# Optimization experiments

Measured on AMD Instinct MI355X. Metric: run time of the kernel, lower is better.

## Reference

```python
import jax, jax.numpy as jnp
import numpy as np

H = 1024      # hidden_size
L = 4         # num_layers
DI = 2 * H    # d_inner (expand=2)
N = 16        # d_state
K = 4         # d_conv
BATCH = 2
S = 1024
EPS = 1e-5


def _layernorm(x, g, b):
    mu = jnp.mean(x, axis=-1, keepdims=True)
    xc = x - mu
    var = jnp.mean(xc * xc, axis=-1, keepdims=True)
    return xc * jax.lax.rsqrt(var + EPS) * g + b


def _causal_dwconv(x, w, b):
    # x: [B,S,DI], w: [DI,K], b: [DI]. Torch Conv1d(pad=K-1, groups=DI) truncated to S == causal left-pad conv.
    xp = jnp.pad(x, ((0, 0), (K - 1, 0), (0, 0)))
    s = x.shape[1]
    y = sum(xp[:, k:k + s, :] * w[:, k] for k in range(K))
    return y + b


def _forward(hidden_states, in_norm_g, in_norm_b, ln_g, ln_b, in_proj_w,
             conv_w, conv_b, x_proj_w, dt_proj_w, dt_proj_b, D,
             mamba_ln_g, mamba_ln_b, out_proj_w, op1_w, op1_b, op2_w, op2_b):
    dtype = hidden_states.dtype
    A = -jnp.arange(1, N + 1, dtype=dtype)  # [N]; == -exp(log(arange)), identical across d_inner rows
    x = _layernorm(hidden_states, in_norm_g, in_norm_b)
    for l in range(L):
        res_x = x
        xn = _layernorm(x, ln_g[l], ln_b[l])
        xr = jnp.einsum('bsh,ph->bsp', xn, in_proj_w[l])           # [B,S,2*DI]
        x_inner, res = jnp.split(xr, 2, axis=-1)
        x_inner = jax.nn.silu(x_inner)
        for c in range(2):
            x_inner = jax.nn.silu(_causal_dwconv(x_inner, conv_w[l, c], conv_b[l, c]))
        proj = jnp.einsum('bsd,pd->bsp', x_inner, x_proj_w[l])     # [B,S,1+2N]
        dt_raw, Bm, Cm = proj[..., :1], proj[..., 1:1 + N], proj[..., 1 + N:]
        dt = jax.nn.softplus(dt_raw * dt_proj_w[l][:, 0] + dt_proj_b[l])  # [B,S,DI]

        def step(h, inp_t):
            dt_t, x_t, B_t, C_t = inp_t                      # [B,DI],[B,DI],[B,N],[B,N]
            h = h + dt_t[..., None] * (h * A + x_t[..., None] * B_t[:, None, :])
            y = jnp.einsum('bdn,bn->bd', h, C_t)
            return h, y

        h0 = jnp.zeros((x.shape[0], DI, N), dtype=dtype)
        xs = (dt.transpose(1, 0, 2), x_inner.transpose(1, 0, 2),
              Bm.transpose(1, 0, 2), Cm.transpose(1, 0, 2))
        _, ys = jax.lax.scan(step, h0, xs)                   # ys: [S,B,DI]
        y = ys.transpose(1, 0, 2)
        y = y + x_inner * D[l]
        y = _layernorm(y, mamba_ln_g[l], mamba_ln_b[l])
        y = y * jax.nn.sigmoid(res)
        x = res_x + jnp.einsum('bsd,hd->bsh', y, out_proj_w[l])
    out = jax.nn.gelu(x @ op1_w.T + op1_b, approximate=False) @ op2_w.T + op2_b
    return out + hidden_states


def setup_inputs() -> dict:
    key = jax.random.key(0)
    ks = jax.random.split(key, 10)
    rn = lambda k, shape, s: jax.random.normal(k, shape, dtype=jnp.float32) * s
    return {
        'hidden_states': rn(ks[0], (BATCH, S, H), 1.0),
        'in_norm_g': jnp.ones((H,), jnp.float32),
        'in_norm_b': jnp.zeros((H,), jnp.float32),
        'ln_g': jnp.ones((L, H), jnp.float32),
        'ln_b': jnp.zeros((L, H), jnp.float32),
        'in_proj_w': rn(ks[1], (L, 2 * DI, H), 0.02),
        'conv_w': rn(ks[2], (L, 2, DI, K), 0.2),
        'conv_b': jnp.zeros((L, 2, DI), jnp.float32),
        'x_proj_w': rn(ks[3], (L, 1 + 2 * N, DI), 0.02),
        'dt_proj_w': rn(ks[4], (L, DI, 1), 0.01),
        'dt_proj_b': jnp.full((L, DI), -4.0, jnp.float32),  # keeps dt small -> stable scan
        'D': jnp.ones((L, DI), jnp.float32),
        'mamba_ln_g': jnp.ones((L, DI), jnp.float32),
        'mamba_ln_b': jnp.zeros((L, DI), jnp.float32),
        'out_proj_w': rn(ks[5], (L, H, DI), 0.02),
        'op1_w': rn(ks[6], (H, H), 0.02),
        'op1_b': jnp.zeros((H,), jnp.float32),
        'op2_w': rn(ks[7], (H, H), 0.02),
        'op2_b': jnp.zeros((H,), jnp.float32),
    }


def reference(hidden_states, in_norm_g, in_norm_b, ln_g, ln_b, in_proj_w,
              conv_w, conv_b, x_proj_w, dt_proj_w, dt_proj_b, D,
              mamba_ln_g, mamba_ln_b, out_proj_w, op1_w, op1_b, op2_w, op2_b):
    return _forward(hidden_states, in_norm_g, in_norm_b, ln_g, ln_b, in_proj_w,
                    conv_w, conv_b, x_proj_w, dt_proj_w, dt_proj_b, D,
                    mamba_ln_g, mamba_ln_b, out_proj_w, op1_w, op1_b, op2_w, op2_b)
```

## Files before the change

### kernel.cpp

```cpp
#include <hip/hip_runtime.h>
#include <hip/hip_bf16.h>
#include <math.h>

constexpr int HDIM = 1024;
constexpr int LNUM = 4;
constexpr int DINNER = 2048;
constexpr int KCONV = 4;
constexpr int NB = 2;
constexpr int SLEN = 1024;
constexpr int TOK = NB * SLEN;
constexpr float LNEPS = 1e-5f;

constexpr int NCHUNK = 32;
constexpr int CLEN = SLEN / NCHUNK;
constexpr int PROW = 36;
constexpr int XPN = 48;
constexpr int XSPLIT = 8;
constexpr int CCH = 32;

typedef __attribute__((ext_vector_type(8))) short short8;
typedef __attribute__((ext_vector_type(4))) float f32x4;

__device__ __forceinline__ __hip_bfloat16 f2bf(float x) { return __float2bfloat16(x); }
__device__ __forceinline__ unsigned short f2bfu(float x) {
    __hip_bfloat16 h = __float2bfloat16(x);
    return *(unsigned short*)&h;
}
__device__ __forceinline__ float sigmoidf_(float x) { return 1.f / (1.f + __expf(-x)); }
__device__ __forceinline__ float siluf_(float x) { return x / (1.f + __expf(-x)); }
__device__ __forceinline__ float softplusf_(float x) { return (x > 20.f) ? x : log1pf(__expf(x)); }

__device__ __forceinline__ void cp16(const void* g, void* l) {
    __builtin_amdgcn_global_load_lds(
        (const __attribute__((address_space(1))) unsigned int*)g,
        (__attribute__((address_space(3))) unsigned int*)l, 16, 0, 0);
}

__global__ __launch_bounds__(256) void cvt_k(const float* __restrict__ in,
                                             __hip_bfloat16* __restrict__ out, int n4)
{
    const int i = blockIdx.x * 256 + threadIdx.x;
    if (i >= n4) return;
    float4 v = ((const float4*)in)[i];
    ushort4 o;
    o.x = f2bfu(v.x); o.y = f2bfu(v.y); o.z = f2bfu(v.z); o.w = f2bfu(v.w);
    ((ushort4*)out)[i] = o;
}

__global__ __launch_bounds__(256) void cvtwx_k(const float* __restrict__ in,
                                               __hip_bfloat16* __restrict__ out)
{
    const int i = blockIdx.x * 256 + threadIdx.x;
    if (i >= LNUM * XPN * DINNER / 4) return;
    const int e = i * 4;
    const int l = e / (XPN * DINNER);
    const int rem = e - l * XPN * DINNER;
    const int r = rem >> 11;
    const int col = rem & (DINNER - 1);
    ushort4 o;
    if (r < 33) {
        float4 v = *(const float4*)&in[(((size_t)l * 33 + r) << 11) + col];
        o.x = f2bfu(v.x); o.y = f2bfu(v.y); o.z = f2bfu(v.z); o.w = f2bfu(v.w);
    } else {
        o.x = o.y = o.z = o.w = 0;
    }
    ((ushort4*)out)[i] = o;
}

template<int MODE, int D>
__global__ __launch_bounds__(256) void ln_k(
    const float* __restrict__ in, const float* __restrict__ g, const float* __restrict__ b,
    float* __restrict__ outF, __hip_bfloat16* __restrict__ outB,
    const float* __restrict__ gate, int gstride)
{
    constexpr int EPT = D / 1024;
    const int t = blockIdx.x, tid = threadIdx.x;
    float4 v[EPT];
    float s1 = 0.f, s2 = 0.f;
#pragma unroll
    for (int i = 0; i < EPT; ++i) {
        const int idx = (tid + i * 256) * 4;
        float4 val = *(const float4*)&in[(size_t)t * D + idx];
        v[i] = val;
        s1 += val.x + val.y + val.z + val.w;
        s2 += val.x * val.x + val.y * val.y + val.z * val.z + val.w * val.w;
    }
#pragma unroll
    for (int off = 32; off; off >>= 1) { s1 += __shfl_down(s1, off); s2 += __shfl_down(s2, off); }
    __shared__ float rs[4], rq[4];
    const int w = tid >> 6, lane = tid & 63;
    if (lane == 0) { rs[w] = s1; rq[w] = s2; }
    __syncthreads();
    const float mu = (rs[0] + rs[1] + rs[2] + rs[3]) * (1.f / D);
    const float ms = (rq[0] + rq[1] + rq[2] + rq[3]) * (1.f / D);
    const float var = ms - mu * mu;
    const float rstd = rsqrtf((var > 0.f ? var : 0.f) + LNEPS);
#pragma unroll
    for (int i = 0; i < EPT; ++i) {
        const int idx = (tid + i * 256) * 4;
        const float4 gg = *(const float4*)&g[idx];
        const float4 bb = *(const float4*)&b[idx];
        float4 o;
        o.x = (v[i].x - mu) * rstd * gg.x + bb.x;
        o.y = (v[i].y - mu) * rstd * gg.y + bb.y;
        o.z = (v[i].z - mu) * rstd * gg.z + bb.z;
        o.w = (v[i].w - mu) * rstd * gg.w + bb.w;
        if (MODE == 2) {
            const float4 gt = *(const float4*)&gate[(size_t)t * gstride + idx];
            o.x *= sigmoidf_(gt.x); o.y *= sigmoidf_(gt.y);
            o.z *= sigmoidf_(gt.z); o.w *= sigmoidf_(gt.w);
        }
        if (MODE == 0) {
            ((float4*)outF)[((size_t)t * D + idx) >> 2] = o;
        } else {
            ushort4 u;
            u.x = f2bfu(o.x); u.y = f2bfu(o.y); u.z = f2bfu(o.z); u.w = f2bfu(o.w);
            ((ushort4*)outB)[((size_t)t * D + idx) >> 2] = u;
        }
    }
}

template<int EPI>
__global__ __launch_bounds__(256) void gemm_bt(
    const unsigned short* __restrict__ A, const unsigned short* __restrict__ B,
    int M, int N, int Kd,
    float* __restrict__ Cf, __hip_bfloat16* __restrict__ Cb,
    const float* __restrict__ bias, const float* __restrict__ res,
    float* __restrict__ Of)
{
    __shared__ __align__(16) unsigned short As[2][128 * 32];
    __shared__ __align__(16) unsigned short Bs[2][128 * 32];
    const int tid = threadIdx.x;
    const int m0 = blockIdx.x * 128, n0 = blockIdx.y * 128;
    const int klen = Kd / (int)gridDim.z;
    const int kstart = (int)blockIdx.z * klen;
    const int nK = klen >> 5;
    const int wave = tid >> 6, lane = tid & 63;
    const int wm = (wave & 1) * 64, wn = (wave >> 1) * 64;
    const int quad = lane >> 4, l16 = lane & 15;
    f32x4 acc[4][4];
#pragma unroll
    for (int i = 0; i < 4; ++i)
#pragma unroll
        for (int j = 0; j < 4; ++j) acc[i][j] = (f32x4){0.f, 0.f, 0.f, 0.f};

    const int r1 = tid >> 2, kc1 = (tid & 3) * 8;
    const int r2 = r1 + 64;

    {
        const int k0 = kstart;
        cp16(&A[(size_t)(m0 + r1) * Kd + k0 + kc1], &As[0][tid * 8]);
        cp16(&A[(size_t)(m0 + r2) * Kd + k0 + kc1], &As[0][(tid + 256) * 8]);
        cp16(&B[(size_t)(n0 + r1) * Kd + k0 + kc1], &Bs[0][tid * 8]);
        cp16(&B[(size_t)(n0 + r2) * Kd + k0 + kc1], &Bs[0][(tid + 256) * 8]);
    }
    for (int kk = 0; kk < nK; ++kk) {
        __syncthreads();
        if (kk + 1 < nK) {
            const int k0 = kstart + ((kk + 1) << 5);
            const int nb = (kk + 1) & 1;
            cp16(&A[(size_t)(m0 + r1) * Kd + k0 + kc1], &As[nb][tid * 8]);
            cp16(&A[(size_t)(m0 + r2) * Kd + k0 + kc1], &As[nb][(tid + 256) * 8]);
            cp16(&B[(size_t)(n0 + r1) * Kd + k0 + kc1], &Bs[nb][tid * 8]);
            cp16(&B[(size_t)(n0 + r2) * Kd + k0 + kc1], &Bs[nb][(tid + 256) * 8]);
        }
        const int cb = kk & 1;
        short8 af[4], bfm[4];
#pragma unroll
        for (int i = 0; i < 4; ++i) af[i]  = *(const short8*)&As[cb][(wm + i * 16 + l16) * 32 + quad * 8];
#pragma unroll
        for (int j = 0; j < 4; ++j) bfm[j] = *(const short8*)&Bs[cb][(wn + j * 16 + l16) * 32 + quad * 8];
#pragma unroll
        for (int i = 0; i < 4; ++i)
#pragma unroll
            for (int j = 0; j < 4; ++j)
                acc[i][j] = __builtin_amdgcn_mfma_f32_16x16x32_bf16(af[i], bfm[j], acc[i][j], 0, 0, 0);
    }

    const size_t zoff = (EPI == 1) ? (size_t)blockIdx.z * M * N : 0;
#pragma unroll
    for (int i = 0; i < 4; ++i)
#pragma unroll
        for (int j = 0; j < 4; ++j)
#pragma unroll
            for (int r = 0; r < 4; ++r) {
                const int row = m0 + wm + i * 16 + quad * 4 + r;
                const int col = n0 + wn + j * 16 + l16;
                const size_t off = (size_t)row * N + col;
                float vv = acc[i][j][r];
                if (EPI == 0) {
                    Cf[off] = vv;
                } else if (EPI == 1) {
                    Cf[zoff + off] = vv;
                } else if (EPI == 2) {
                    float z = vv + bias[col];
                    Cb[off] = f2bf(0.5f * z * (1.f + erff(z * 0.70710678118f)));
                } else {
                    Of[off] = vv + bias[col] + res[off];
                }
            }
}

__global__ __launch_bounds__(256) void xcomb_k(const float* __restrict__ part,
                                               float* __restrict__ x, int n4)
{
    const int i = blockIdx.x * 256 + threadIdx.x;
    if (i >= n4) return;
    float4 a = ((const float4*)part)[i];
    float4 b = ((const float4*)part)[i + n4];
    float4 v = ((const float4*)x)[i];
    v.x += a.x + b.x; v.y += a.y + b.y; v.z += a.z + b.z; v.w += a.w + b.w;
    ((float4*)x)[i] = v;
}

__global__ __launch_bounds__(256) void pcomb_k(const float* __restrict__ ppart,
                                               float* __restrict__ proj)
{
    const int idx = blockIdx.x * 256 + threadIdx.x;
    if (idx >= TOK * 33) return;
    const int t = idx / 33, p2 = idx - t * 33;
    float s = 0.f;
#pragma unroll
    for (int k = 0; k < XSPLIT; ++k)
        s += ppart[(size_t)k * TOK * XPN + (size_t)t * XPN + p2];
    proj[idx] = s;
}

__global__ __launch_bounds__(256) void conv2_fused(
    const float* __restrict__ xin, int in_stride,
    const float* __restrict__ cw, const float* __restrict__ cb, int layer,
    float* __restrict__ out, __hip_bfloat16* __restrict__ outb)
{
    const int d = blockIdx.x * 256 + threadIdx.x;
    const int s0 = blockIdx.y * CCH;
    const int b = blockIdx.z;
    float w1k[4], w2k[4];
#pragma unroll
    for (int k = 0; k < 4; ++k) {
        w1k[k] = cw[(((size_t)layer * 2 + 0) * DINNER + d) * KCONV + k];
        w2k[k] = cw[(((size_t)layer * 2 + 1) * DINNER + d) * KCONV + k];
    }
    const float b1 = cb[((size_t)layer * 2 + 0) * DINNER + d];
    const float b2 = cb[((size_t)layer * 2 + 1) * DINNER + d];
    const float* base = xin + (size_t)b * SLEN * in_stride + d;

    float xv[CCH + 6];
#pragma unroll
    for (int i = 0; i < CCH + 6; ++i) {
        const int s = s0 - 6 + i;
        const int sc = (s < 0) ? 0 : s;
        xv[i] = base[(size_t)sc * in_stride];
    }
#pragma unroll
    for (int i = 0; i < CCH + 6; ++i) {
        const int s = s0 - 6 + i;
        xv[i] = (s >= 0) ? siluf_(xv[i]) : 0.f;
    }
    float c1[CCH + 3];
#pragma unroll
    for (int i = 0; i < CCH + 3; ++i) {
        const int s = s0 - 3 + i;
        float t = fmaf(w1k[0], xv[i], fmaf(w1k[1], xv[i + 1],
                  fmaf(w1k[2], xv[i + 2], fmaf(w1k[3], xv[i + 3], b1))));
        c1[i] = (s >= 0) ? siluf_(t) : 0.f;
    }
    const size_t obase = (size_t)b * SLEN * DINNER + d;
#pragma unroll
    for (int j = 0; j < CCH; ++j) {
        float t2 = fmaf(w2k[0], c1[j], fmaf(w2k[1], c1[j + 1],
                   fmaf(w2k[2], c1[j + 2], fmaf(w2k[3], c1[j + 3], b2))));
        const float v = siluf_(t2);
        out[obase + (size_t)(s0 + j) * DINNER] = v;
        outb[obase + (size_t)(s0 + j) * DINNER] = f2bf(v);
    }
}

__global__ __launch_bounds__(256) void xproj_mfma(
    const unsigned short* __restrict__ A, const unsigned short* __restrict__ B,
    float* __restrict__ ppart)
{
    __shared__ __align__(16) unsigned short As[2][128 * 32];
    __shared__ __align__(16) unsigned short Bs[2][XPN * 32];
    const int tid = threadIdx.x;
    const int m0 = blockIdx.x * 128;
    const int k0base = blockIdx.y * (DINNER / XSPLIT);
    constexpr int nK = (DINNER / XSPLIT) >> 5;
    const int wave = tid >> 6, lane = tid & 63;
    const int wm = wave * 32;
    const int quad = lane >> 4, l16 = lane & 15;
    f32x4 acc[2][3];
#pragma unroll
    for (int i = 0; i < 2; ++i)
#pragma unroll
        for (int j = 0; j < 3; ++j) acc[i][j] = (f32x4){0.f, 0.f, 0.f, 0.f};

    const int r1 = tid >> 2, kc1 = (tid & 3) * 8;
    {
        const int k0 = k0base;
        cp16(&A[(size_t)(m0 + r1) * DINNER + k0 + kc1], &As[0][tid * 8]);
        cp16(&A[(size_t)(m0 + r1 + 64) * DINNER + k0 + kc1], &As[0][(tid + 256) * 8]);
        if (tid < XPN * 4)
            cp16(&B[(size_t)r1 * DINNER + k0 + kc1], &Bs[0][tid * 8]);
    }
    for (int kk = 0; kk < nK; ++kk) {
        __syncthreads();
        if (kk + 1 < nK) {
            const int k0 = k0base + ((kk + 1) << 5);
            const int nb = (kk + 1) & 1;
            cp16(&A[(size_t)(m0 + r1) * DINNER + k0 + kc1], &As[nb][tid * 8]);
            cp16(&A[(size_t)(m0 + r1 + 64) * DINNER + k0 + kc1], &As[nb][(tid + 256) * 8]);
            if (tid < XPN * 4)
                cp16(&B[(size_t)r1 * DINNER + k0 + kc1], &Bs[nb][tid * 8]);
        }
        const int cb = kk & 1;
        short8 af[2], bfm[3];
#pragma unroll
        for (int i = 0; i < 2; ++i) af[i]  = *(const short8*)&As[cb][(wm + i * 16 + l16) * 32 + quad * 8];
#pragma unroll
        for (int j = 0; j < 3; ++j) bfm[j] = *(const short8*)&Bs[cb][(j * 16 + l16) * 32 + quad * 8];
#pragma unroll
        for (int i = 0; i < 2; ++i)
#pragma unroll
            for (int j = 0; j < 3; ++j)
                acc[i][j] = __builtin_amdgcn_mfma_f32_16x16x32_bf16(af[i], bfm[j], acc[i][j], 0, 0, 0);
    }
    float* pp = ppart + (size_t)blockIdx.y * TOK * XPN;
#pragma unroll
    for (int i = 0; i < 2; ++i)
#pragma unroll
        for (int j = 0; j < 3; ++j) {
            const int col = j * 16 + l16;
#pragma unroll
            for (int r = 0; r < 4; ++r) {
                const int row = m0 + wm + i * 16 + quad * 4 + r;
                pp[(size_t)row * XPN + col] = acc[i][j][r];
            }
        }
}

__device__ __forceinline__ void load_proj_chunk(float* sp, const float* __restrict__ proj,
                                                int b, int c, int tid)
{
    const float* psrc = proj + ((size_t)b * SLEN + (size_t)c * CLEN) * 33;
    for (int i = tid; i < CLEN * 33; i += 256) {
        int s = i / 33, p = i - s * 33;
        sp[s * PROW + (p == 0 ? 32 : p - 1)] = psrc[i];
    }
}

__global__ __launch_bounds__(256) void scan_partA(
    const float* __restrict__ proj, const float* __restrict__ xin,
    const float* __restrict__ dtw, const float* __restrict__ dtb, int layer,
    float* __restrict__ hloc, float* __restrict__ cumA_g)
{
    __shared__ __align__(16) float sp[CLEN * PROW];
    const int tid = threadIdx.x;
    const int d = blockIdx.x * 256 + tid;
    const int c = blockIdx.y, b = blockIdx.z;
    load_proj_chunk(sp, proj, b, c, tid);
    const float w_ = dtw[(size_t)layer * DINNER + d];
    const float bb = dtb[(size_t)layer * DINNER + d];
    __syncthreads();
    float h[16], ca[16];
#pragma unroll
    for (int n = 0; n < 16; ++n) { h[n] = 0.f; ca[n] = 1.f; }
    const float* xrow = xin + ((size_t)b * SLEN + (size_t)c * CLEN) * DINNER + d;
    float xt_next = xrow[0];
    for (int s = 0; s < CLEN; ++s) {
        const float xt = xt_next;
        if (s + 1 < CLEN) xt_next = xrow[(size_t)(s + 1) * DINNER];
        const float* row = &sp[s * PROW];
        const float dt = softplusf_(fmaf(row[32], w_, bb));
        const float u = dt * xt;
#pragma unroll
        for (int n = 0; n < 16; ++n) {
            const float a = fmaf(dt, -(float)(n + 1), 1.f);
            h[n] = fmaf(h[n], a, u * row[n]);
            ca[n] *= a;
        }
    }
    const size_t base = (((size_t)b * NCHUNK + c) * 16) * DINNER + d;
#pragma unroll
    for (int n = 0; n < 16; ++n) {
        hloc[base + (size_t)n * DINNER] = h[n];
        cumA_g[base + (size_t)n * DINNER] = ca[n];
    }
}

__global__ __launch_bounds__(256) void scan_combine(
    const float* __restrict__ hloc, const float* __restrict__ cumA_g,
    float* __restrict__ hin)
{
    const int idx = blockIdx.x * 256 + threadIdx.x;
    const int d = idx & (DINNER - 1);
    const int n = (idx >> 11) & 15;
    const int b = idx >> 15;
    float h = 0.f;
    for (int c = 0; c < NCHUNK; ++c) {
        const size_t off = (((size_t)b * NCHUNK + c) * 16 + n) * DINNER + d;
        hin[off] = h;
        h = fmaf(cumA_g[off], h, hloc[off]);
    }
}

__global__ __launch_bounds__(256) void scan_partC(
    const float* __restrict__ proj, const float* __restrict__ xin,
    const float* __restrict__ dtw, const float* __restrict__ dtb,
    const float* __restrict__ Dp, int layer,
    const float* __restrict__ hin, float* __restrict__ y)
{
    __shared__ __align__(16) float sp[CLEN * PROW];
    const int tid = threadIdx.x;
    const int d = blockIdx.x * 256 + tid;
    const int c = blockIdx.y, b = blockIdx.z;
    load_proj_chunk(sp, proj, b, c, tid);
    const float w_ = dtw[(size_t)layer * DINNER + d];
    const float bb = dtb[(size_t)layer * DINNER + d];
    const float Dd = Dp[(size_t)layer * DINNER + d];
    __syncthreads();
    float h[16];
    const size_t base = (((size_t)b * NCHUNK + c) * 16) * DINNER + d;
#pragma unroll
    for (int n = 0; n < 16; ++n) h[n] = hin[base + (size_t)n * DINNER];
    const float* xrow = xin + ((size_t)b * SLEN + (size_t)c * CLEN) * DINNER + d;
    float* yrow = y + ((size_t)b * SLEN + (size_t)c * CLEN) * DINNER + d;
    float xt_next = xrow[0];
    for (int s = 0; s < CLEN; ++s) {
        const float xt = xt_next;
        if (s + 1 < CLEN) xt_next = xrow[(size_t)(s + 1) * DINNER];
        const float* row = &sp[s * PROW];
        const float dt = softplusf_(fmaf(row[32], w_, bb));
        const float u = dt * xt;
        float yp = 0.f;
#pragma unroll
        for (int n = 0; n < 16; ++n) {
            const float a = fmaf(dt, -(float)(n + 1), 1.f);
            h[n] = fmaf(h[n], a, u * row[n]);
            yp = fmaf(h[n], row[16 + n], yp);
        }
        yrow[(size_t)s * DINNER] = yp + xt * Dd;
    }
}

__global__ __launch_bounds__(256) void cast_f2b(const float* __restrict__ in,
                                                __hip_bfloat16* __restrict__ out, int n4)
{
    int i = blockIdx.x * 256 + threadIdx.x;
    if (i >= n4) return;
    float4 v = ((const float4*)in)[i];
    ushort4 u;
    u.x = f2bfu(v.x); u.y = f2bfu(v.y); u.z = f2bfu(v.z); u.w = f2bfu(v.w);
    ((ushort4*)out)[i] = u;
}

extern "C" void kernel_launch(void* const* d_in, const int* in_sizes, int n_in,
                              void* d_out, int out_size, void* d_ws, size_t ws_size,
                              hipStream_t stream)
{
    (void)in_sizes; (void)n_in; (void)out_size;
    const float* hs   = (const float*)d_in[0];
    const float* ing  = (const float*)d_in[1];
    const float* inb  = (const float*)d_in[2];
    const float* lng  = (const float*)d_in[3];
    const float* lnb  = (const float*)d_in[4];
    const float* ipw  = (const float*)d_in[5];
    const float* cw   = (const float*)d_in[6];
    const float* cbp  = (const float*)d_in[7];
    const float* xpw  = (const float*)d_in[8];
    const float* dtw  = (const float*)d_in[9];
    const float* dtb  = (const float*)d_in[10];
    const float* Dp   = (const float*)d_in[11];
    const float* mlg  = (const float*)d_in[12];
    const float* mlb  = (const float*)d_in[13];
    const float* opw  = (const float*)d_in[14];
    const float* w1f  = (const float*)d_in[15];
    const float* b1f  = (const float*)d_in[16];
    const float* w2f  = (const float*)d_in[17];
    const float* b2f  = (const float*)d_in[18];

    char* p = (char*)d_ws;
    float* x   = (float*)p; p += (size_t)TOK * HDIM * 4;
    float* xr  = (float*)p; p += (size_t)TOK * 2 * DINNER * 4;
    float* c2  = (float*)p; p += (size_t)TOK * DINNER * 4;
    float* yb  = (float*)p; p += (size_t)TOK * DINNER * 4;
    float* proj= (float*)p; p += ((size_t)TOK * 33 * 4 + 255) & ~(size_t)255;
    float* hin = (float*)p; p += (size_t)NB * NCHUNK * 16 * DINNER * 4;
    float* ppart=(float*)p; p += (size_t)XSPLIT * TOK * XPN * 4;
    __hip_bfloat16* xn  = (__hip_bfloat16*)p; p += (size_t)TOK * HDIM * 2;
    __hip_bfloat16* y2  = (__hip_bfloat16*)p; p += (size_t)TOK * DINNER * 2;
    __hip_bfloat16* c2b = (__hip_bfloat16*)p; p += (size_t)TOK * DINNER * 2;
    __hip_bfloat16* wx  = (__hip_bfloat16*)p; p += (size_t)LNUM * XPN * DINNER * 2;
    __hip_bfloat16* t1 = (__hip_bfloat16*)xr;
    float* hloc = yb;
    float* cumA = yb + (size_t)NB * NCHUNK * 16 * DINNER;
    float* opart = c2;

    const size_t IPL = (size_t)2 * DINNER * HDIM;
    const size_t OPL = (size_t)HDIM * DINNER;
    const size_t MLPW = (size_t)HDIM * HDIM;

    size_t used = (size_t)(p - (char*)d_ws);
    const bool bulk = (used + (IPL * LNUM + OPL * LNUM + 2 * MLPW) * 2) <= ws_size;

    __hip_bfloat16 *wi[LNUM], *wo[LNUM], *w1, *w2;
    if (bulk) {
        for (int l = 0; l < LNUM; ++l) { wi[l] = (__hip_bfloat16*)p; p += IPL * 2; }
        for (int l = 0; l < LNUM; ++l) { wo[l] = (__hip_bfloat16*)p; p += OPL * 2; }
        w1 = (__hip_bfloat16*)p; p += MLPW * 2;
        w2 = (__hip_bfloat16*)p; p += MLPW * 2;
    } else {
        __hip_bfloat16* slotA = (__hip_bfloat16*)p; p += IPL * 2;
        __hip_bfloat16* slotB = (__hip_bfloat16*)p; p += OPL * 2;
        for (int l = 0; l < LNUM; ++l) { wi[l] = slotA; wo[l] = slotB; }
        w1 = slotA; w2 = slotB;
    }

    cvtwx_k<<<(LNUM * XPN * DINNER / 4 + 255) / 256, 256, 0, stream>>>(xpw, wx);

    if (bulk) {
        cvt_k<<<(int)(IPL * LNUM / 4 / 256), 256, 0, stream>>>(ipw, wi[0], (int)(IPL * LNUM / 4));
        cvt_k<<<(int)(OPL * LNUM / 4 / 256), 256, 0, stream>>>(opw, wo[0], (int)(OPL * LNUM / 4));
        cvt_k<<<(int)(MLPW / 4 / 256), 256, 0, stream>>>(w1f, w1, (int)(MLPW / 4));
        cvt_k<<<(int)(MLPW / 4 / 256), 256, 0, stream>>>(w2f, w2, (int)(MLPW / 4));
    }

    ln_k<0, HDIM><<<TOK, 256, 0, stream>>>(hs, ing, inb, x, nullptr, nullptr, 0);

    for (int l = 0; l < LNUM; ++l) {
        ln_k<1, HDIM><<<TOK, 256, 0, stream>>>(x, lng + (size_t)l * HDIM, lnb + (size_t)l * HDIM,
                                               nullptr, xn, nullptr, 0);
        if (!bulk)
            cvt_k<<<(int)(IPL / 4 / 256), 256, 0, stream>>>(ipw + (size_t)l * IPL, wi[l], (int)(IPL / 4));
        gemm_bt<0><<<dim3(TOK / 128, (2 * DINNER) / 128), 256, 0, stream>>>(
            (const unsigned short*)xn, (const unsigned short*)wi[l],
            TOK, 2 * DINNER, HDIM, xr, nullptr, nullptr, nullptr, nullptr);

        conv2_fused<<<dim3(DINNER / 256, SLEN / CCH, NB), 256, 0, stream>>>(
            xr, 2 * DINNER, cw, cbp, l, c2, c2b);

        xproj_mfma<<<dim3(TOK / 128, XSPLIT), 256, 0, stream>>>(
            (const unsigned short*)c2b, (const unsigned short*)(wx + (size_t)l * XPN * DINNER), ppart);
        pcomb_k<<<(TOK * 33 + 255) / 256, 256, 0, stream>>>(ppart, proj);

        scan_partA<<<dim3(DINNER / 256, NCHUNK, NB), 256, 0, stream>>>(
            proj, c2, dtw, dtb, l, hloc, cumA);
        scan_combine<<<(NB * 16 * DINNER) / 256, 256, 0, stream>>>(hloc, cumA, hin);
        scan_partC<<<dim3(DINNER / 256, NCHUNK, NB), 256, 0, stream>>>(
            proj, c2, dtw, dtb, Dp, l, hin, yb);

        ln_k<2, DINNER><<<TOK, 256, 0, stream>>>(yb, mlg + (size_t)l * DINNER, mlb + (size_t)l * DINNER,
                                                 nullptr, y2, xr + DINNER, 2 * DINNER);

        if (!bulk)
            cvt_k<<<(int)(OPL / 4 / 256), 256, 0, stream>>>(opw + (size_t)l * OPL, wo[l], (int)(OPL / 4));
        gemm_bt<1><<<dim3(TOK / 128, HDIM / 128, 2), 256, 0, stream>>>(
            (const unsigned short*)y2, (const unsigned short*)wo[l],
            TOK, HDIM, DINNER, opart, nullptr, nullptr, nullptr, nullptr);
        xcomb_k<<<(TOK * HDIM / 4 + 255) / 256, 256, 0, stream>>>(opart, x, TOK * HDIM / 4);
    }

    cast_f2b<<<(TOK * HDIM / 4 + 255) / 256, 256, 0, stream>>>(x, xn, TOK * HDIM / 4);
    if (!bulk) {
        cvt_k<<<(int)(MLPW / 4 / 256), 256, 0, stream>>>(w1f, w1, (int)(MLPW / 4));
        cvt_k<<<(int)(MLPW / 4 / 256), 256, 0, stream>>>(w2f, w2, (int)(MLPW / 4));
    }
    gemm_bt<2><<<dim3(TOK / 128, HDIM / 128), 256, 0, stream>>>(
        (const unsigned short*)xn, (const unsigned short*)w1,
        TOK, HDIM, HDIM, nullptr, t1, b1f, nullptr, nullptr);
    gemm_bt<3><<<dim3(TOK / 128, HDIM / 128), 256, 0, stream>>>(
        (const unsigned short*)t1, (const unsigned short*)w2,
        TOK, HDIM, HDIM, nullptr, nullptr, b2f, hs, (float*)d_out);
}
```

Measured before the change: 874.0 us.

## Fuse residual combine with next-layer LayerNorm and fold x_proj reduction into scan

Merges the split-K residual combine with the following layer's LayerNorm into one per-token kernel. On the last layer it merges the combine with the final bf16 cast. It also removes the pcomb_k kernel, so the scan kernels now sum the x_proj split-K partials while loading each chunk, and doubles XSPLIT to 16 for more xproj parallelism. This cuts kernel launches and intermediate round-trips through global memory. In exchange, partA and partC each re-sum 16 partials per element, and LayerNorm now uses a one-pass E[x^2]-mu^2 variance.

```diff
diff --git a/kernel.cpp b/kernel.cpp
--- a/kernel.cpp
+++ b/kernel.cpp
@@ -15,7 +15,7 @@
 constexpr int CLEN = SLEN / NCHUNK;
 constexpr int PROW = 36;
 constexpr int XPN = 48;
-constexpr int XSPLIT = 8;
+constexpr int XSPLIT = 16;
 constexpr int CCH = 32;
 
 typedef __attribute__((ext_vector_type(8))) short short8;
@@ -118,6 +118,56 @@
             ((ushort4*)outB)[((size_t)t * D + idx) >> 2] = u;
         }
     }
+}
+
+__global__ __launch_bounds__(256) void xcomb_ln_k(
+    const float* __restrict__ part, float* __restrict__ x,
+    const float* __restrict__ g, const float* __restrict__ b,
+    __hip_bfloat16* __restrict__ outB)
+{
+    const int t = blockIdx.x, tid = threadIdx.x;
+    const int idx = tid * 4;
+    const size_t off = (size_t)t * HDIM + idx;
+    float4 a = *(const float4*)&part[off];
+    float4 c = *(const float4*)&part[(size_t)TOK * HDIM + off];
+    float4 v = *(const float4*)&x[off];
+    v.x += a.x + c.x; v.y += a.y + c.y; v.z += a.z + c.z; v.w += a.w + c.w;
+    *(float4*)&x[off] = v;
+    float s1 = v.x + v.y + v.z + v.w;
+    float s2 = v.x * v.x + v.y * v.y + v.z * v.z + v.w * v.w;
+#pragma unroll
+    for (int o2 = 32; o2; o2 >>= 1) { s1 += __shfl_down(s1, o2); s2 += __shfl_down(s2, o2); }
+    __shared__ float rs[4], rq[4];
+    const int w = tid >> 6, lane = tid & 63;
+    if (lane == 0) { rs[w] = s1; rq[w] = s2; }
+    __syncthreads();
+    const float mu = (rs[0] + rs[1] + rs[2] + rs[3]) * (1.f / HDIM);
+    const float ms = (rq[0] + rq[1] + rq[2] + rq[3]) * (1.f / HDIM);
+    const float var = ms - mu * mu;
+    const float rstd = rsqrtf((var > 0.f ? var : 0.f) + LNEPS);
+    const float4 gg = *(const float4*)&g[idx];
+    const float4 bb = *(const float4*)&b[idx];
+    ushort4 u;
+    u.x = f2bfu((v.x - mu) * rstd * gg.x + bb.x);
+    u.y = f2bfu((v.y - mu) * rstd * gg.y + bb.y);
+    u.z = f2bfu((v.z - mu) * rstd * gg.z + bb.z);
+    u.w = f2bfu((v.w - mu) * rstd * gg.w + bb.w);
+    ((ushort4*)outB)[off >> 2] = u;
+}
+
+__global__ __launch_bounds__(256) void xcomb_cast_k(
+    const float* __restrict__ part, const float* __restrict__ x,
+    __hip_bfloat16* __restrict__ xn, int n4)
+{
+    const int i = blockIdx.x * 256 + threadIdx.x;
+    if (i >= n4) return;
+    float4 a = ((const float4*)part)[i];
+    float4 c = ((const float4*)part)[i + n4];
+    float4 v = ((const float4*)x)[i];
+    v.x += a.x + c.x; v.y += a.y + c.y; v.z += a.z + c.z; v.w += a.w + c.w;
+    ushort4 u;
+    u.x = f2bfu(v.x); u.y = f2bfu(v.y); u.z = f2bfu(v.z); u.w = f2bfu(v.w);
+    ((ushort4*)xn)[i] = u;
 }
 
 template<int EPI>
@@ -201,31 +251,6 @@
             }
 }
 
-__global__ __launch_bounds__(256) void xcomb_k(const float* __restrict__ part,
-                                               float* __restrict__ x, int n4)
-{
-    const int i = blockIdx.x * 256 + threadIdx.x;
-    if (i >= n4) return;
-    float4 a = ((const float4*)part)[i];
-    float4 b = ((const float4*)part)[i + n4];
-    float4 v = ((const float4*)x)[i];
-    v.x += a.x + b.x; v.y += a.y + b.y; v.z += a.z + b.z; v.w += a.w + b.w;
-    ((float4*)x)[i] = v;
-}
-
-__global__ __launch_bounds__(256) void pcomb_k(const float* __restrict__ ppart,
-                                               float* __restrict__ proj)
-{
-    const int idx = blockIdx.x * 256 + threadIdx.x;
-    if (idx >= TOK * 33) return;
-    const int t = idx / 33, p2 = idx - t * 33;
-    float s = 0.f;
-#pragma unroll
-    for (int k = 0; k < XSPLIT; ++k)
-        s += ppart[(size_t)k * TOK * XPN + (size_t)t * XPN + p2];
-    proj[idx] = s;
-}
-
 __global__ __launch_bounds__(256) void conv2_fused(
     const float* __restrict__ xin, int in_stride,
     const float* __restrict__ cw, const float* __restrict__ cb, int layer,
@@ -338,18 +363,22 @@
         }
 }
 
-__device__ __forceinline__ void load_proj_chunk(float* sp, const float* __restrict__ proj,
+__device__ __forceinline__ void load_proj_chunk(float* sp, const float* __restrict__ ppart,
                                                 int b, int c, int tid)
 {
-    const float* psrc = proj + ((size_t)b * SLEN + (size_t)c * CLEN) * 33;
+    const int t0 = b * SLEN + c * CLEN;
     for (int i = tid; i < CLEN * 33; i += 256) {
         int s = i / 33, p = i - s * 33;
-        sp[s * PROW + (p == 0 ? 32 : p - 1)] = psrc[i];
+        float sum = 0.f;
+#pragma unroll
+        for (int k = 0; k < XSPLIT; ++k)
+            sum += ppart[(size_t)k * TOK * XPN + (size_t)(t0 + s) * XPN + p];
+        sp[s * PROW + (p == 0 ? 32 : p - 1)] = sum;
     }
 }
 
 __global__ __launch_bounds__(256) void scan_partA(
-    const float* __restrict__ proj, const float* __restrict__ xin,
+    const float* __restrict__ ppart, const float* __restrict__ xin,
     const float* __restrict__ dtw, const float* __restrict__ dtb, int layer,
     float* __restrict__ hloc, float* __restrict__ cumA_g)
 {
@@ -357,7 +386,7 @@
     const int tid = threadIdx.x;
     const int d = blockIdx.x * 256 + tid;
     const int c = blockIdx.y, b = blockIdx.z;
-    load_proj_chunk(sp, proj, b, c, tid);
+    load_proj_chunk(sp, ppart, b, c, tid);
     const float w_ = dtw[(size_t)layer * DINNER + d];
     const float bb = dtb[(size_t)layer * DINNER + d];
     __syncthreads();
@@ -404,7 +433,7 @@
 }
 
 __global__ __launch_bounds__(256) void scan_partC(
-    const float* __restrict__ proj, const float* __restrict__ xin,
+    const float* __restrict__ ppart, const float* __restrict__ xin,
     const float* __restrict__ dtw, const float* __restrict__ dtb,
     const float* __restrict__ Dp, int layer,
     const float* __restrict__ hin, float* __restrict__ y)
@@ -413,7 +442,7 @@
     const int tid = threadIdx.x;
     const int d = blockIdx.x * 256 + tid;
     const int c = blockIdx.y, b = blockIdx.z;
-    load_proj_chunk(sp, proj, b, c, tid);
+    load_proj_chunk(sp, ppart, b, c, tid);
     const float w_ = dtw[(size_t)layer * DINNER + d];
     const float bb = dtb[(size_t)layer * DINNER + d];
     const float Dd = Dp[(size_t)layer * DINNER + d];
@@ -440,17 +469,6 @@
         }
         yrow[(size_t)s * DINNER] = yp + xt * Dd;
     }
-}
-
-__global__ __launch_bounds__(256) void cast_f2b(const float* __restrict__ in,
-                                                __hip_bfloat16* __restrict__ out, int n4)
-{
-    int i = blockIdx.x * 256 + threadIdx.x;
-    if (i >= n4) return;
-    float4 v = ((const float4*)in)[i];
-    ushort4 u;
-    u.x = f2bfu(v.x); u.y = f2bfu(v.y); u.z = f2bfu(v.z); u.w = f2bfu(v.w);
-    ((ushort4*)out)[i] = u;
 }
 
 extern "C" void kernel_launch(void* const* d_in, const int* in_sizes, int n_in,
@@ -483,7 +501,6 @@
     float* xr  = (float*)p; p += (size_t)TOK * 2 * DINNER * 4;
     float* c2  = (float*)p; p += (size_t)TOK * DINNER * 4;
     float* yb  = (float*)p; p += (size_t)TOK * DINNER * 4;
-    float* proj= (float*)p; p += ((size_t)TOK * 33 * 4 + 255) & ~(size_t)255;
     float* hin = (float*)p; p += (size_t)NB * NCHUNK * 16 * DINNER * 4;
     float* ppart=(float*)p; p += (size_t)XSPLIT * TOK * XPN * 4;
     __hip_bfloat16* xn  = (__hip_bfloat16*)p; p += (size_t)TOK * HDIM * 2;
@@ -525,10 +542,9 @@
     }
 
     ln_k<0, HDIM><<<TOK, 256, 0, stream>>>(hs, ing, inb, x, nullptr, nullptr, 0);
+    ln_k<1, HDIM><<<TOK, 256, 0, stream>>>(x, lng, lnb, nullptr, xn, nullptr, 0);
 
     for (int l = 0; l < LNUM; ++l) {
-        ln_k<1, HDIM><<<TOK, 256, 0, stream>>>(x, lng + (size_t)l * HDIM, lnb + (size_t)l * HDIM,
-                                               nullptr, xn, nullptr, 0);
         if (!bulk)
             cvt_k<<<(int)(IPL / 4 / 256), 256, 0, stream>>>(ipw + (size_t)l * IPL, wi[l], (int)(IPL / 4));
         gemm_bt<0><<<dim3(TOK / 128, (2 * DINNER) / 128), 256, 0, stream>>>(
@@ -540,13 +556,12 @@
 
         xproj_mfma<<<dim3(TOK / 128, XSPLIT), 256, 0, stream>>>(
             (const unsigned short*)c2b, (const unsigned short*)(wx + (size_t)l * XPN * DINNER), ppart);
-        pcomb_k<<<(TOK * 33 + 255) / 256, 256, 0, stream>>>(ppart, proj);
 
         scan_partA<<<dim3(DINNER / 256, NCHUNK, NB), 256, 0, stream>>>(
-            proj, c2, dtw, dtb, l, hloc, cumA);
+            ppart, c2, dtw, dtb, l, hloc, cumA);
         scan_combine<<<(NB * 16 * DINNER) / 256, 256, 0, stream>>>(hloc, cumA, hin);
         scan_partC<<<dim3(DINNER / 256, NCHUNK, NB), 256, 0, stream>>>(
-            proj, c2, dtw, dtb, Dp, l, hin, yb);
+            ppart, c2, dtw, dtb, Dp, l, hin, yb);
 
         ln_k<2, DINNER><<<TOK, 256, 0, stream>>>(yb, mlg + (size_t)l * DINNER, mlb + (size_t)l * DINNER,
                                                  nullptr, y2, xr + DINNER, 2 * DINNER);
@@ -556,10 +571,15 @@
         gemm_bt<1><<<dim3(TOK / 128, HDIM / 128, 2), 256, 0, stream>>>(
             (const unsigned short*)y2, (const unsigned short*)wo[l],
             TOK, HDIM, DINNER, opart, nullptr, nullptr, nullptr, nullptr);
-        xcomb_k<<<(TOK * HDIM / 4 + 255) / 256, 256, 0, stream>>>(opart, x, TOK * HDIM / 4);
-    }
-
-    cast_f2b<<<(TOK * HDIM / 4 + 255) / 256, 256, 0, stream>>>(x, xn, TOK * HDIM / 4);
+        if (l + 1 < LNUM) {
+            xcomb_ln_k<<<TOK, 256, 0, stream>>>(opart, x,
+                lng + (size_t)(l + 1) * HDIM, lnb + (size_t)(l + 1) * HDIM, xn);
+        } else {
+            xcomb_cast_k<<<(TOK * HDIM / 4 + 255) / 256, 256, 0, stream>>>(
+                opart, x, xn, TOK * HDIM / 4);
+        }
+    }
+
     if (!bulk) {
         cvt_k<<<(int)(MLPW / 4 / 256), 256, 0, stream>>>(w1f, w1, (int)(MLPW / 4));
         cvt_k<<<(int)(MLPW / 4 / 256), 256, 0, stream>>>(w2f, w2, (int)(MLPW / 4));
```

New measurement: 890.2 us. No clear change (+1.9%).
